# Optimization experiments

Measured on AMD Instinct MI355X. Metric: run time of the kernel, lower is better.

Reference implementation:

```python
import jax, jax.numpy as jnp
import numpy as np

DIM = 256
NUM_HEADS = 8
NUM_NEI = (16, 32)
G = len(NUM_NEI)          # branches
G_H = NUM_HEADS // G      # heads per branch = 4
G_DIM = DIM // G          # channels per branch = 128
HD = G_DIM // G_H         # head dim = 32
SCALE = HD ** (-0.5)
M_MSF = G                 # MSF branches
CHANNEL = DIM // M_MSF    # 128
D_MSF = CHANNEL           # r=1

gelu = lambda t: jax.nn.gelu(t, approximate=False)


def setup_inputs() -> dict:
    key = jax.random.key(0)
    ks = jax.random.split(key, 16)
    B, N = 4, 2048
    s = lambda fan: fan ** (-0.5)
    inp = {
        "x": jax.random.normal(ks[0], (B, N, DIM), jnp.float32),
        "pos": jax.random.uniform(ks[1], (B, N, 3), jnp.float32),
        # qkv linear (no bias); stored as (in, out)
        "Wqkv": jax.random.normal(ks[2], (DIM, 3 * DIM), jnp.float32) * s(DIM),
        # per-branch rel-pos MLPs: Linear(3, g_dim) + GELU
        "Wp0": jax.random.normal(ks[3], (3, G_DIM), jnp.float32) * s(3),
        "bp0": jnp.zeros((G_DIM,), jnp.float32),
        "Wp1": jax.random.normal(ks[4], (3, G_DIM), jnp.float32) * s(3),
        "bp1": jnp.zeros((G_DIM,), jnp.float32),
        # MSF params
        "W_proj": jax.random.normal(ks[5], (DIM, DIM), jnp.float32) * s(DIM),
        "b_proj": jnp.zeros((DIM,), jnp.float32),
        "W_fc1": jax.random.normal(ks[6], (DIM, D_MSF), jnp.float32) * s(DIM),
        "b_fc1": jnp.zeros((D_MSF,), jnp.float32),
        "W_fc2": jax.random.normal(ks[7], (D_MSF, M_MSF * CHANNEL), jnp.float32) * s(D_MSF),
        "b_fc2": jnp.zeros((M_MSF * CHANNEL,), jnp.float32),
        "W_head": jax.random.normal(ks[8], (DIM, DIM), jnp.float32) * s(DIM),
        "b_head": jnp.zeros((DIM,), jnp.float32),
    }
    return inp


def _branch(q, k, v, pos, knn_idx, Wp, bp):
    """One head-group: KNN gather + rel-pos MLP fused attention.
    q,k,v: [B,N,g_dim]; pos: [B,N,3]; knn_idx: [B,N,nk]."""
    B, N, g_dim = k.shape
    nk = knn_idx.shape[-1]
    gather = jax.vmap(lambda t, idx: t[idx])  # per-batch fancy gather -> [B,N,nk,D]
    knn_xyz = gather(pos, knn_idx)                       # [B,N,nk,3]
    kg = gather(k, knn_idx)                              # [B,N,nk,g_dim]
    vg = gather(v, knn_idx)
    # split heads: b n k (h d) -> b h n k d
    split = lambda t: t.reshape(B, N, nk, G_H, HD).transpose(0, 3, 1, 2, 4)
    kg, vg = split(kg), split(vg)
    rel = pos[:, :, None, :] - knn_xyz                   # [B,N,nk,3]
    vrp = split(gelu(rel @ Wp + bp))                     # [B,h,N,nk,d]
    vg = vg + vrp
    attn_rel = vrp.sum(-1)                               # [B,h,N,nk]
    qh = q.reshape(B, N, G_H, HD).transpose(0, 2, 1, 3)  # [B,h,N,d]
    logits = jnp.einsum('bhnd,bhnkd->bhnk', qh, kg) * SCALE + attn_rel
    a = jax.nn.softmax(logits, axis=-1)
    out = jnp.einsum('bhnk,bhnkd->bhnd', a, vg)          # [B,h,N,d]
    return out.transpose(0, 2, 1, 3).reshape(B, N, g_dim)


def _msf(x, W_proj, b_proj, W_fc1, b_fc1, W_fc2, b_fc2, W_head, b_head):
    bs, N, dim = x.shape
    input_groups = x.transpose(0, 2, 1).reshape(bs, M_MSF, CHANNEL, N)
    feats_proj = gelu(x @ W_proj + b_proj)               # [bs,N,dim]
    feats_S = feats_proj.mean(axis=1)                    # global avg pool over N -> [bs,dim]
    feats_Z = gelu(feats_S @ W_fc1 + b_fc1)
    av = (feats_Z @ W_fc2 + b_fc2).reshape(bs, M_MSF, CHANNEL, 1)
    av = jax.nn.softmax(av, axis=1)                      # softmax over branches
    feats_V = (input_groups * av).reshape(bs, dim, N).transpose(0, 2, 1)
    feats_V = feats_V @ W_head + b_head
    return feats_proj + feats_V


def reference(x, pos, Wqkv, Wp0, bp0, Wp1, bp1,
              W_proj, b_proj, W_fc1, b_fc1, W_fc2, b_fc2, W_head, b_head):
    B, N, C = x.shape
    # pairwise squared distances [B,N,N] (broadcast form, as in source)
    dists = jnp.sum((pos[:, :, None, :] - pos[:, None, :, :]) ** 2, axis=-1)
    order = jnp.argsort(dists, axis=-1)                  # [B,N,N]
    qkv = (x @ Wqkv).reshape(B, N, 3, C).transpose(2, 0, 1, 3)  # [3,B,N,C]
    pos_params = [(Wp0, bp0), (Wp1, bp1)]
    outs = []
    for i, nk in enumerate(NUM_NEI):
        sl = slice(i * G_DIM, (i + 1) * G_DIM)
        q, k, v = qkv[0][..., sl], qkv[1][..., sl], qkv[2][..., sl]
        knn_idx = order[:, :, :nk]
        Wp, bp = pos_params[i]
        outs.append(_branch(q, k, v, pos, knn_idx, Wp, bp))
    xcat = jnp.concatenate(outs, axis=-1)                # [B,N,C]
    return _msf(xcat, W_proj, b_proj, W_fc1, b_fc1, W_fc2, b_fc2, W_head, b_head)
```

## Files before the change

kernel.cpp:

```cpp
#include <hip/hip_runtime.h>
#include <cstdint>
#include <cstddef>

#define B_    4
#define NPT   2048
#define DIM_  256
#define QKVW  768
#define XLEN  2097152
#define QLEN  196608
#define PLEN  65536
#define TOTC  (XLEN + QLEN + 2 * PLEN)

typedef unsigned short ushort_t;
typedef unsigned long long u64;
typedef short bf16x8 __attribute__((ext_vector_type(8)));
typedef float f32x4 __attribute__((ext_vector_type(4)));

__device__ __forceinline__ float gelu_f(float x) {
  return 0.5f * x * (1.0f + erff(x * 0.70710678118654752440f));
}

__device__ __forceinline__ float gelu_fast(float x) {
  const float is2 = 0.70710678118654752440f;
  float z = x * is2;
  float az = __builtin_fabsf(z);
  float t = __builtin_amdgcn_rcpf(fmaf(0.3275911f, az, 1.0f));
  float p = fmaf(1.061405429f, t, -1.453152027f);
  p = fmaf(p, t, 1.421413741f);
  p = fmaf(p, t, -0.284496736f);
  p = fmaf(p, t, 0.254829592f);
  p = p * t;
  float e = __expf(-az * az);
  float er = fmaf(-p, e, 1.0f);
  er = __builtin_copysignf(er, x);
  return 0.5f * x * (1.0f + er);
}

__device__ __forceinline__ ushort_t f2bf(float f) {
  unsigned u = __float_as_uint(f);
  unsigned r = (u + 0x7fffu + ((u >> 16) & 1u)) >> 16;
  return (ushort_t)r;
}
__device__ __forceinline__ float bf2f(ushort_t h) {
  return __uint_as_float(((unsigned)h) << 16);
}

template <int CTRL>
__device__ __forceinline__ float dpp_addf(float x) {
  int s = __builtin_amdgcn_update_dpp(0, __float_as_int(x), CTRL, 0xf, 0xf, false);
  return x + __int_as_float(s);
}
template <int CTRL>
__device__ __forceinline__ int dpp_addi(int x) {
  int s = __builtin_amdgcn_update_dpp(0, x, CTRL, 0xf, 0xf, false);
  return x + s;
}
__device__ __forceinline__ int wave_sum_i(int x) {
  x = dpp_addi<0x111>(x);
  x = dpp_addi<0x112>(x);
  x = dpp_addi<0x114>(x);
  x = dpp_addi<0x118>(x);
  x = dpp_addi<0x142>(x);
  x = dpp_addi<0x143>(x);
  return x;
}

__device__ __forceinline__ float bfly16_sum(float x) {
  x += __int_as_float(__builtin_amdgcn_ds_swizzle(__float_as_int(x), 0x041F));
  x += __int_as_float(__builtin_amdgcn_ds_swizzle(__float_as_int(x), 0x081F));
  x += __int_as_float(__builtin_amdgcn_ds_swizzle(__float_as_int(x), 0x101F));
  x += __int_as_float(__builtin_amdgcn_ds_swizzle(__float_as_int(x), 0x201F));
  return x;
}

__device__ __forceinline__ bf16x8 scale_bf(bf16x8 v, const float* avk) {
  bf16x8 r;
#pragma unroll
  for (int e = 0; e < 8; e++) {
    float f = bf2f((ushort_t)v[e]) * avk[e];
    r[e] = (short)f2bf(f);
  }
  return r;
}

__global__ __launch_bounds__(256) void convert_kernel(
    const float* __restrict__ x, const float* __restrict__ Wqkv,
    const float* __restrict__ Wproj, const float* __restrict__ Whead,
    ushort_t* __restrict__ xbf, ushort_t* __restrict__ WqkvT,
    ushort_t* __restrict__ WprojT, ushort_t* __restrict__ WheadT,
    float* __restrict__ part) {
  int base = blockIdx.x * 256 + threadIdx.x;
  if (base < 1024) part[base] = 0.f;
  for (int i = base; i < TOTC; i += 2048 * 256) {
    if (i < XLEN) {
      xbf[i] = f2bf(x[i]);
    } else if (i < XLEN + QLEN) {
      int e = i - XLEN;
      int k = e / 768, n = e - k * 768;
      WqkvT[n * 256 + k] = f2bf(Wqkv[e]);
    } else if (i < XLEN + QLEN + PLEN) {
      int e = i - XLEN - QLEN;
      int k = e >> 8, n = e & 255;
      WprojT[n * 256 + k] = f2bf(Wproj[e]);
    } else {
      int e = i - XLEN - QLEN - PLEN;
      int k = e >> 8, n = e & 255;
      WheadT[n * 256 + k] = f2bf(Whead[e]);
    }
  }
}

__global__ __launch_bounds__(64, 4) void knn_gemm0_kernel(
    const float* __restrict__ pos, int* __restrict__ idx_out,
    const ushort_t* __restrict__ A, const ushort_t* __restrict__ BT,
    float* __restrict__ C) {
  __shared__ u64 buf[128];
  __shared__ unsigned cnt;
  int lane = threadIdx.x;
  if (blockIdx.x >= 8192) {
    constexpr int K = 256;
    constexpr int N = 768;
    int quad = lane >> 4, r16 = lane & 15;
    int t0 = blockIdx.x - 8192;
    int m0 = (t0 / 24) * 64, n0 = (t0 % 24) * 32;
    const ushort_t* Ap = A + (size_t)(m0 + r16) * K + quad * 8;
    const ushort_t* Bp = BT + (size_t)(n0 + r16) * K + quad * 8;
    f32x4 acc[4][2] = {};
    bf16x8 af[4], bfv[2], af2[4], bf2[2];
#pragma unroll
    for (int i = 0; i < 4; i++) af[i] = *(const bf16x8*)(Ap + (size_t)i * 16 * K);
#pragma unroll
    for (int j = 0; j < 2; j++) bfv[j] = *(const bf16x8*)(Bp + (size_t)j * 16 * K);
#pragma unroll
    for (int kc = 0; kc < 8; kc++) {
      if (kc < 7) {
        int ko = (kc + 1) * 32;
#pragma unroll
        for (int i = 0; i < 4; i++)
          af2[i] = *(const bf16x8*)(Ap + (size_t)i * 16 * K + ko);
#pragma unroll
        for (int j = 0; j < 2; j++)
          bf2[j] = *(const bf16x8*)(Bp + (size_t)j * 16 * K + ko);
      }
#pragma unroll
      for (int i = 0; i < 4; i++) {
        acc[i][0] = __builtin_amdgcn_mfma_f32_16x16x32_bf16(af[i], bfv[0], acc[i][0], 0, 0, 0);
        acc[i][1] = __builtin_amdgcn_mfma_f32_16x16x32_bf16(af[i], bfv[1], acc[i][1], 0, 0, 0);
      }
#pragma unroll
      for (int i = 0; i < 4; i++) af[i] = af2[i];
      bfv[0] = bf2[0]; bfv[1] = bf2[1];
    }
#pragma unroll
    for (int i = 0; i < 4; i++) {
#pragma unroll
      for (int j = 0; j < 2; j++) {
        int col = n0 + j * 16 + r16;
#pragma unroll
        for (int r = 0; r < 4; r++) {
          int row = m0 + i * 16 + quad * 4 + r;
          C[(size_t)row * N + col] = acc[i][j][r];
        }
      }
    }
    return;
  }
  int wq = blockIdx.x;
  int b = wq >> 11, n = wq & (NPT - 1);
  const float* pb = pos + (size_t)b * NPT * 3;
  float qx = pb[n * 3 + 0], qy = pb[n * 3 + 1], qz = pb[n * 3 + 2];
  u64 keys[32];
  {
#pragma clang fp contract(off)
#pragma unroll
    for (int s = 0; s < 32; s++) {
      int j = lane + (s << 6);
      float dx = qx - pb[j * 3 + 0];
      float dy = qy - pb[j * 3 + 1];
      float dz = qz - pb[j * 3 + 2];
      float d = dx * dx;
      d = d + dy * dy;
      d = d + dz * dz;
      keys[s] = ((u64)__float_as_uint(d) << 32) | (unsigned)j;
    }
  }
  unsigned lo = 0, hi = 0x40400001u;
  for (int it = 0; it < 31 && hi - lo > 1; ++it) {
    unsigned mid = (lo + hi) >> 1;
    int c = 0;
#pragma unroll
    for (int s = 0; s < 32; s++)
      c += ((unsigned)(keys[s] >> 32) < mid) ? 1 : 0;
    c = __builtin_amdgcn_readlane(wave_sum_i(c), 63);
    if (c >= 32) { hi = mid; if (c <= 64) break; }
    else lo = mid;
  }
  unsigned T = hi;
  buf[lane] = ~0ULL;
  buf[lane + 64] = ~0ULL;
  if (lane == 0) cnt = 0;
  __builtin_amdgcn_wave_barrier();
  asm volatile("s_waitcnt lgkmcnt(0)" ::: "memory");
  int cl = 0;
#pragma unroll
  for (int s = 0; s < 32; s++)
    cl += ((unsigned)(keys[s] >> 32) < T) ? 1 : 0;
  unsigned base = atomicAdd(&cnt, (unsigned)cl);
  unsigned w = base;
#pragma unroll
  for (int s = 0; s < 32; s++) {
    if ((unsigned)(keys[s] >> 32) < T && w < 128) {
      buf[w] = keys[s];
      w++;
    }
  }
  __builtin_amdgcn_wave_barrier();
  asm volatile("s_waitcnt lgkmcnt(0)" ::: "memory");
  unsigned total = cnt;
  total = (unsigned)__builtin_amdgcn_readfirstlane((int)total);
  if (total > 128u) total = 128u;
  unsigned mt = (total + 7u) & ~7u;
  u64 k0 = buf[lane];
  u64 k1 = buf[lane + 64];
  int r0 = 0, r1 = 0;
  for (unsigned i = 0; i < mt; i += 8) {
#pragma unroll
    for (int t = 0; t < 8; t++) {
      u64 ki = buf[i + t];
      r0 += (ki < k0) ? 1 : 0;
      r1 += (ki < k1) ? 1 : 0;
    }
  }
  if (r0 < 32) idx_out[(size_t)wq * 32 + r0] = (int)(unsigned)(k0 & 0xffffffffULL);
  if (r1 < 32) idx_out[(size_t)wq * 32 + r1] = (int)(unsigned)(k1 & 0xffffffffULL);
}

template <int MODE>
__global__ __launch_bounds__(64, 4) void gemm_rf(
    const ushort_t* __restrict__ A, const ushort_t* __restrict__ BT,
    const float* __restrict__ bias, const float* __restrict__ extra,
    float* __restrict__ C, float* __restrict__ part,
    const float* __restrict__ av, int N) {
  constexpr int K = 256;
  int lane = threadIdx.x;
  int quad = lane >> 4, r16 = lane & 15;
  int t0 = blockIdx.x;
  int m0 = (t0 >> 3) * 64, n0 = (t0 & 7) * 32;
  int batch = m0 >> 11;
  const ushort_t* Ap = A + (size_t)(m0 + r16) * K + quad * 8;
  const ushort_t* Bp = BT + (size_t)(n0 + r16) * K + quad * 8;
  f32x4 acc[4][2] = {};
  bf16x8 af[4], bf[2], af2[4], bf2[2];
#pragma unroll
  for (int i = 0; i < 4; i++) af[i] = *(const bf16x8*)(Ap + (size_t)i * 16 * K);
#pragma unroll
  for (int j = 0; j < 2; j++) bf[j] = *(const bf16x8*)(Bp + (size_t)j * 16 * K);
#pragma unroll
  for (int kc = 0; kc < 8; kc++) {
    if (kc < 7) {
      int ko = (kc + 1) * 32;
#pragma unroll
      for (int i = 0; i < 4; i++)
        af2[i] = *(const bf16x8*)(Ap + (size_t)i * 16 * K + ko);
#pragma unroll
      for (int j = 0; j < 2; j++)
        bf2[j] = *(const bf16x8*)(Bp + (size_t)j * 16 * K + ko);
    }
    bf16x8 b0 = bf[0], b1 = bf[1];
    if (MODE == 2) {
      const float* avk = av + batch * 256 + kc * 32 + quad * 8;
      b0 = scale_bf(b0, avk);
      b1 = scale_bf(b1, avk);
    }
#pragma unroll
    for (int i = 0; i < 4; i++) {
      acc[i][0] = __builtin_amdgcn_mfma_f32_16x16x32_bf16(af[i], b0, acc[i][0], 0, 0, 0);
      acc[i][1] = __builtin_amdgcn_mfma_f32_16x16x32_bf16(af[i], b1, acc[i][1], 0, 0, 0);
    }
#pragma unroll
    for (int i = 0; i < 4; i++) af[i] = af2[i];
    bf[0] = bf2[0]; bf[1] = bf2[1];
  }
  float cs[2] = {};
#pragma unroll
  for (int i = 0; i < 4; i++) {
#pragma unroll
    for (int j = 0; j < 2; j++) {
      int col = n0 + j * 16 + r16;
#pragma unroll
      for (int r = 0; r < 4; r++) {
        int row = m0 + i * 16 + quad * 4 + r;
        float v = acc[i][j][r];
        if (MODE == 1) { v = gelu_fast(v + bias[col]); cs[j] += v; }
        else if (MODE == 2) v = extra[(size_t)row * 256 + col] + v + bias[col];
        C[(size_t)row * N + col] = v;
      }
    }
  }
  if (MODE == 1) {
#pragma unroll
    for (int j = 0; j < 2; j++) {
      cs[j] += __shfl_xor(cs[j], 16, 64);
      cs[j] += __shfl_xor(cs[j], 32, 64);
    }
    if (quad == 0) {
#pragma unroll
      for (int j = 0; j < 2; j++)
        atomicAdd(&part[batch * 256 + n0 + j * 16 + r16], cs[j]);
    }
  }
}

template <int NK>
__device__ __forceinline__ void attn_core(
    const float* __restrict__ kvbase, int c2, const int* sidx,
    const float4* srel, float qSx, float qSy,
    float2 w0, float2 w1, float2 w2, float2 bb,
    float& num0, float& num1, float& den) {
#pragma unroll
  for (int j = 0; j < NK; j++) {
    int jj = __builtin_amdgcn_readfirstlane(sidx[j]);
    float4 rr = srel[j];
    const float* kb = kvbase + (size_t)jj * QKVW;
    float2 kv = *(const float2*)(kb + c2);
    float2 vv = *(const float2*)(kb + 256 + c2);
    float x0 = fmaf(rr.x, w0.x, fmaf(rr.y, w1.x, fmaf(rr.z, w2.x, bb.x)));
    float x1 = fmaf(rr.x, w0.y, fmaf(rr.y, w1.y, fmaf(rr.z, w2.y, bb.y)));
    float z0 = x0 * fmaf(0.0713548163f, x0 * x0, 1.5957691216f);
    float z1 = x1 * fmaf(0.0713548163f, x1 * x1, 1.5957691216f);
    float r0 = x0 * __builtin_amdgcn_rcpf(1.0f + __expf(-z0));
    float r1 = x1 * __builtin_amdgcn_rcpf(1.0f + __expf(-z1));
    float p = fmaf(qSx, kv.x, r0) + fmaf(qSy, kv.y, r1);
    float logit = bfly16_sum(p);
    float e = __expf(logit);
    den += e;
    num0 = fmaf(e, vv.x + r0, num0);
    num1 = fmaf(e, vv.y + r1, num1);
  }
}

__global__ __launch_bounds__(64) void attn_kernel(
    const float* __restrict__ qkv, const float* __restrict__ pos,
    const int* __restrict__ knn,
    const float* __restrict__ Wp0, const float* __restrict__ bp0,
    const float* __restrict__ Wp1, const float* __restrict__ bp1,
    ushort_t* __restrict__ xcat) {
  const float SCALE = 0.17677669529663687f;
  int u = blockIdx.x;
  int g = blockIdx.y;
  int b = u >> 11, n = u & (NPT - 1);
  int lane = threadIdx.x;
  int c2 = lane * 2;
  __shared__ int s_idx[32];
  __shared__ float4 s_rel[32];
  const float* qkvb = qkv + (size_t)b * NPT * QKVW;
  if (lane < 32) {
    int j = knn[(size_t)u * 32 + lane];
    s_idx[lane] = j;
    const float* pn = pos + ((size_t)b * NPT + n) * 3;
    const float* pj = pos + ((size_t)b * NPT + j) * 3;
    s_rel[lane] = make_float4(pn[0] - pj[0], pn[1] - pj[1],
                              pn[2] - pj[2], 0.f);
  }
  __builtin_amdgcn_wave_barrier();
  asm volatile("s_waitcnt lgkmcnt(0)" ::: "memory");
  const float* Wp = g ? Wp1 : Wp0;
  const float* bp = g ? bp1 : bp0;
  float2 w0 = *(const float2*)(Wp + c2);
  float2 w1 = *(const float2*)(Wp + 128 + c2);
  float2 w2 = *(const float2*)(Wp + 256 + c2);
  float2 bb = *(const float2*)(bp + c2);
  float2 q2 = *(const float2*)(qkvb + (size_t)n * QKVW + g * 128 + c2);
  float qSx = q2.x * SCALE, qSy = q2.y * SCALE;
  const float* kvbase = qkvb + 256 + g * 128;
  float num0 = 0.f, num1 = 0.f, den = 0.f;
  if (g == 0)
    attn_core<16>(kvbase, c2, s_idx, s_rel, qSx, qSy, w0, w1, w2, bb,
                  num0, num1, den);
  else
    attn_core<32>(kvbase, c2, s_idx, s_rel, qSx, qSy, w0, w1, w2, bb,
                  num0, num1, den);
  float inv = __builtin_amdgcn_rcpf(den);
  unsigned pk = (unsigned)f2bf(num0 * inv) | ((unsigned)f2bf(num1 * inv) << 16);
  ((unsigned*)xcat)[((size_t)b * NPT + n) * 128 + g * 64 + lane] = pk;
}

__global__ __launch_bounds__(256) void msf_av_kernel(
    const float* __restrict__ part, const float* __restrict__ Wfc1,
    const float* __restrict__ bfc1, const float* __restrict__ Wfc2,
    const float* __restrict__ bfc2, float* __restrict__ av_out) {
  int b = blockIdx.x, t = threadIdx.x;
  __shared__ float S[256], Z[128], A[256];
  S[t] = part[b * 256 + t] * (1.0f / 2048.0f);
  __syncthreads();
  if (t < 128) {
    float z = bfc1[t];
    for (int i = 0; i < 256; i++) z += S[i] * Wfc1[i * 128 + t];
    Z[t] = gelu_f(z);
  }
  __syncthreads();
  float a = bfc2[t];
  for (int j = 0; j < 128; j++) a += Z[j] * Wfc2[j * 256 + t];
  A[t] = a;
  __syncthreads();
  float pA = A[t ^ 128];
  float m = fmaxf(a, pA);
  float e = expf(a - m);
  av_out[b * 256 + t] = e / (e + expf(pA - m));
}

extern "C" void kernel_launch(void* const* d_in, const int* in_sizes, int n_in,
                              void* d_out, int out_size, void* d_ws, size_t ws_size,
                              hipStream_t stream) {
  const float* x     = (const float*)d_in[0];
  const float* pos   = (const float*)d_in[1];
  const float* Wqkv  = (const float*)d_in[2];
  const float* Wp0   = (const float*)d_in[3];
  const float* bp0   = (const float*)d_in[4];
  const float* Wp1   = (const float*)d_in[5];
  const float* bp1   = (const float*)d_in[6];
  const float* Wproj = (const float*)d_in[7];
  const float* bproj = (const float*)d_in[8];
  const float* Wfc1  = (const float*)d_in[9];
  const float* bfc1  = (const float*)d_in[10];
  const float* Wfc2  = (const float*)d_in[11];
  const float* bfc2  = (const float*)d_in[12];
  const float* Whead = (const float*)d_in[13];
  const float* bhead = (const float*)d_in[14];
  float* out = (float*)d_out;

  char* ws = (char*)d_ws;
  size_t off = 0;
  int* idx = (int*)(ws + off);              off += (size_t)B_ * NPT * 32 * 4;
  float* qkv = (float*)(ws + off);          off += (size_t)B_ * NPT * QKVW * 4;
  float* fp = qkv;
  ushort_t* xbf = (ushort_t*)(ws + off);    off += (size_t)B_ * NPT * DIM_ * 2;
  ushort_t* xcat = xbf;
  ushort_t* WqkvT = (ushort_t*)(ws + off);  off += (size_t)QLEN * 2;
  ushort_t* WprojT = (ushort_t*)(ws + off); off += (size_t)PLEN * 2;
  ushort_t* WheadT = (ushort_t*)(ws + off); off += (size_t)PLEN * 2;
  float* part = (float*)(ws + off);         off += 1024 * 4;
  float* av = (float*)(ws + off);           off += 1024 * 4;

  const int M = B_ * NPT;

  convert_kernel<<<2048, 256, 0, stream>>>(x, Wqkv, Wproj, Whead,
                                           xbf, WqkvT, WprojT, WheadT, part);
  knn_gemm0_kernel<<<8192 + 3072, 64, 0, stream>>>(pos, idx, xbf, WqkvT, qkv);
  attn_kernel<<<dim3(M, 2), 64, 0, stream>>>(qkv, pos, idx,
                                             Wp0, bp0, Wp1, bp1, xcat);
  gemm_rf<1><<<1024, 64, 0, stream>>>(xcat, WprojT, bproj, nullptr,
                                      fp, part, nullptr, DIM_);
  msf_av_kernel<<<B_, 256, 0, stream>>>(part, Wfc1, bfc1, Wfc2, bfc2, av);
  gemm_rf<2><<<1024, 64, 0, stream>>>(xcat, WheadT, bhead, fp,
                                      out, nullptr, av, DIM_);
}
```

Before: 190.5 us.

## Pack four KNN waves per block and use ballot-based counting and compaction

The KNN+QKV-GEMM kernel now runs four waves per 256-thread block instead of one wave per block, with each wave owning a private slice of shared memory. Distances are held as 32-bit floats rather than packed 64-bit keys, which roughly halves register use. The threshold bisection counts candidates with ballot/popcount instead of a DPP reduction, and the candidate compaction uses mbcnt prefix offsets instead of an LDS atomic. The goal is less launch and scheduling overhead, higher occupancy and fewer LDS atomics, at the cost of ballot work on every bisection step.

```diff
diff --git a/kernel.cpp b/kernel.cpp
--- a/kernel.cpp
+++ b/kernel.cpp
@@ -43,26 +43,6 @@
 }
 __device__ __forceinline__ float bf2f(ushort_t h) {
   return __uint_as_float(((unsigned)h) << 16);
-}
-
-template <int CTRL>
-__device__ __forceinline__ float dpp_addf(float x) {
-  int s = __builtin_amdgcn_update_dpp(0, __float_as_int(x), CTRL, 0xf, 0xf, false);
-  return x + __int_as_float(s);
-}
-template <int CTRL>
-__device__ __forceinline__ int dpp_addi(int x) {
-  int s = __builtin_amdgcn_update_dpp(0, x, CTRL, 0xf, 0xf, false);
-  return x + s;
-}
-__device__ __forceinline__ int wave_sum_i(int x) {
-  x = dpp_addi<0x111>(x);
-  x = dpp_addi<0x112>(x);
-  x = dpp_addi<0x114>(x);
-  x = dpp_addi<0x118>(x);
-  x = dpp_addi<0x142>(x);
-  x = dpp_addi<0x143>(x);
-  return x;
 }
 
 __device__ __forceinline__ float bfly16_sum(float x) {
@@ -110,18 +90,18 @@
   }
 }
 
-__global__ __launch_bounds__(64, 4) void knn_gemm0_kernel(
+__global__ __launch_bounds__(256, 6) void knn_gemm0_kernel(
     const float* __restrict__ pos, int* __restrict__ idx_out,
     const ushort_t* __restrict__ A, const ushort_t* __restrict__ BT,
     float* __restrict__ C) {
-  __shared__ u64 buf[128];
-  __shared__ unsigned cnt;
-  int lane = threadIdx.x;
-  if (blockIdx.x >= 8192) {
+  __shared__ u64 buf[4][128];
+  int tid = threadIdx.x;
+  int w = tid >> 6, lane = tid & 63;
+  if (blockIdx.x >= 2048) {
     constexpr int K = 256;
     constexpr int N = 768;
     int quad = lane >> 4, r16 = lane & 15;
-    int t0 = blockIdx.x - 8192;
+    int t0 = (blockIdx.x - 2048) * 4 + w;
     int m0 = (t0 / 24) * 64, n0 = (t0 % 24) * 32;
     const ushort_t* Ap = A + (size_t)(m0 + r16) * K + quad * 8;
     const ushort_t* Bp = BT + (size_t)(n0 + r16) * K + quad * 8;
@@ -165,11 +145,11 @@
     }
     return;
   }
-  int wq = blockIdx.x;
+  int wq = blockIdx.x * 4 + w;
   int b = wq >> 11, n = wq & (NPT - 1);
   const float* pb = pos + (size_t)b * NPT * 3;
   float qx = pb[n * 3 + 0], qy = pb[n * 3 + 1], qz = pb[n * 3 + 2];
-  u64 keys[32];
+  float dist[32];
   {
 #pragma clang fp contract(off)
 #pragma unroll
@@ -181,52 +161,51 @@
       float d = dx * dx;
       d = d + dy * dy;
       d = d + dz * dz;
-      keys[s] = ((u64)__float_as_uint(d) << 32) | (unsigned)j;
+      dist[s] = d;
     }
   }
   unsigned lo = 0, hi = 0x40400001u;
   for (int it = 0; it < 31 && hi - lo > 1; ++it) {
     unsigned mid = (lo + hi) >> 1;
+    float fm = __uint_as_float(mid);
     int c = 0;
 #pragma unroll
     for (int s = 0; s < 32; s++)
-      c += ((unsigned)(keys[s] >> 32) < mid) ? 1 : 0;
-    c = __builtin_amdgcn_readlane(wave_sum_i(c), 63);
+      c += (int)__popcll(__ballot(dist[s] < fm));
     if (c >= 32) { hi = mid; if (c <= 64) break; }
     else lo = mid;
   }
-  unsigned T = hi;
-  buf[lane] = ~0ULL;
-  buf[lane + 64] = ~0ULL;
-  if (lane == 0) cnt = 0;
+  float fT = __uint_as_float(hi);
+  buf[w][lane] = ~0ULL;
+  buf[w][lane + 64] = ~0ULL;
   __builtin_amdgcn_wave_barrier();
   asm volatile("s_waitcnt lgkmcnt(0)" ::: "memory");
-  int cl = 0;
-#pragma unroll
-  for (int s = 0; s < 32; s++)
-    cl += ((unsigned)(keys[s] >> 32) < T) ? 1 : 0;
-  unsigned base = atomicAdd(&cnt, (unsigned)cl);
-  unsigned w = base;
+  unsigned base = 0;
 #pragma unroll
   for (int s = 0; s < 32; s++) {
-    if ((unsigned)(keys[s] >> 32) < T && w < 128) {
-      buf[w] = keys[s];
-      w++;
-    }
+    bool m = dist[s] < fT;
+    u64 bal = __ballot(m);
+    unsigned pre = __builtin_amdgcn_mbcnt_hi(
+        (unsigned)(bal >> 32), __builtin_amdgcn_mbcnt_lo((unsigned)bal, 0u));
+    unsigned p = base + pre;
+    if (m && p < 128u) {
+      int j = lane + (s << 6);
+      buf[w][p] = ((u64)__float_as_uint(dist[s]) << 32) | (unsigned)j;
+    }
+    base += (unsigned)__popcll(bal);
   }
   __builtin_amdgcn_wave_barrier();
   asm volatile("s_waitcnt lgkmcnt(0)" ::: "memory");
-  unsigned total = cnt;
-  total = (unsigned)__builtin_amdgcn_readfirstlane((int)total);
+  unsigned total = base;
   if (total > 128u) total = 128u;
   unsigned mt = (total + 7u) & ~7u;
-  u64 k0 = buf[lane];
-  u64 k1 = buf[lane + 64];
+  u64 k0 = buf[w][lane];
+  u64 k1 = buf[w][lane + 64];
   int r0 = 0, r1 = 0;
   for (unsigned i = 0; i < mt; i += 8) {
 #pragma unroll
     for (int t = 0; t < 8; t++) {
-      u64 ki = buf[i + t];
+      u64 ki = buf[w][i + t];
       r0 += (ki < k0) ? 1 : 0;
       r1 += (ki < k1) ? 1 : 0;
     }
@@ -446,7 +425,7 @@
 
   convert_kernel<<<2048, 256, 0, stream>>>(x, Wqkv, Wproj, Whead,
                                            xbf, WqkvT, WprojT, WheadT, part);
-  knn_gemm0_kernel<<<8192 + 3072, 64, 0, stream>>>(pos, idx, xbf, WqkvT, qkv);
+  knn_gemm0_kernel<<<2048 + 768, 256, 0, stream>>>(pos, idx, xbf, WqkvT, qkv);
   attn_kernel<<<dim3(M, 2), 64, 0, stream>>>(qkv, pos, idx,
                                              Wp0, bp0, Wp1, bp1, xcat);
   gemm_rf<1><<<1024, 64, 0, stream>>>(xcat, WprojT, bproj, nullptr,
```

New measurement: 191.8 us. No clear change (+0.7%).
